# Performance work log

Hardware: AMD Instinct MI355X
Metric: run time of the kernel (lower is better)

Reference implementation:

```python
import jax, jax.numpy as jnp
import numpy as np

B, T, C, H, HD = 4, 2048, 1024, 16, 64

def setup_inputs() -> dict:
    key = jax.random.key(0)
    ks = jax.random.split(key, 9)
    s = 1.0 / np.sqrt(C)
    return {
        "x":  jax.random.normal(ks[0], (B, T, C), jnp.float32),
        "Wq": jax.random.normal(ks[1], (H, C, HD), jnp.float32) * s,
        "bq": jax.random.normal(ks[2], (H, HD), jnp.float32) * 0.02,
        "Wk": jax.random.normal(ks[3], (H, C, HD), jnp.float32) * s,
        "bk": jax.random.normal(ks[4], (H, HD), jnp.float32) * 0.02,
        "Wv": jax.random.normal(ks[5], (H, C, HD), jnp.float32) * s,
        "bv": jax.random.normal(ks[6], (H, HD), jnp.float32) * 0.02,
        "Wo": jax.random.normal(ks[7], (C, C), jnp.float32) * s,
        "bo": jax.random.normal(ks[8], (C,), jnp.float32) * 0.02,
    }

def reference(x, Wq, bq, Wk, bk, Wv, bv, Wo, bo):
    # Batched per-head linear projections: [B,T,C] x [H,C,D] -> [B,H,T,D]
    q = jnp.einsum('btc,hcd->bhtd', x, Wq) + bq[None, :, None, :]
    k = jnp.einsum('btc,hcd->bhtd', x, Wk) + bk[None, :, None, :]
    v = jnp.einsum('btc,hcd->bhtd', x, Wv) + bv[None, :, None, :]
    scale = 1.0 / jnp.sqrt(jnp.asarray(HD, q.dtype))
    scores = jnp.einsum('bhtd,bhsd->bhts', q, k) * scale  # [B,H,T,T]
    causal = jnp.tril(jnp.ones((T, T), dtype=bool))
    scores = jnp.where(causal[None, None, :, :], scores, -jnp.inf)
    attn = jax.nn.softmax(scores, axis=-1)
    out = jnp.einsum('bhts,bhsd->bhtd', attn, v)          # [B,H,T,D]
    concat = out.transpose(0, 2, 1, 3).reshape(B, T, C)   # concat heads
    return concat @ Wo + bo
```

## Files before the change

kernel.cpp:

```cpp
#include <hip/hip_runtime.h>
#include <stdint.h>

#define TSEQ 2048
#define NHEAD 16

typedef __attribute__((ext_vector_type(8))) short bf16x8;
typedef __attribute__((ext_vector_type(4))) short bf16x4;
typedef __attribute__((ext_vector_type(4))) float f32x4;

__device__ __forceinline__ unsigned short f2bf(float f) {
  union { float f; uint32_t u; } c;
  c.f = f;
  uint32_t u = c.u;
  u += 0x7fffu + ((u >> 16) & 1u);
  return (unsigned short)(u >> 16);
}

__device__ __forceinline__ float fexp2(float x) {
#if __has_builtin(__builtin_amdgcn_exp2f)
  return __builtin_amdgcn_exp2f(x);
#else
  return __builtin_exp2f(x);
#endif
}

using as3_void  = __attribute__((address_space(3))) void;
using as1_cvoid = const __attribute__((address_space(1))) void;

__device__ __forceinline__ void gld_lds16(const void* g, void* l) {
  __builtin_amdgcn_global_load_lds((as1_cvoid*)g, (as3_void*)l, 16, 0, 0);
}


__global__ void cast_x_kernel(const float4* __restrict__ x, unsigned short* __restrict__ xb) {
  int i = blockIdx.x * 256 + threadIdx.x;
  float4 v = x[i];
  int e = i * 4;
  int m = e >> 10, k = e & 1023;
  int ks = k ^ ((m & 7) << 3);
  ushort4 o;
  o.x = f2bf(v.x); o.y = f2bf(v.y); o.z = f2bf(v.z); o.w = f2bf(v.w);
  *(ushort4*)(xb + (size_t)m * 1024 + ks) = o;
}

__global__ void repack_wqkv(const float* __restrict__ Wq, const float* __restrict__ Wk,
                            const float* __restrict__ Wv, unsigned short* __restrict__ BT) {
  __shared__ unsigned short tile[64][72];
  const float* W = (blockIdx.z == 0) ? Wq : (blockIdx.z == 1) ? Wk : Wv;
  const int h = blockIdx.y;
  const int c0 = blockIdx.x * 64;
  const int t = threadIdx.x;
  const float* src = W + ((size_t)h * 1024 + c0) * 64;
#pragma unroll
  for (int p = 0; p < 16; ++p) {
    int idx = p * 256 + t;
    int cc = idx >> 6, d = idx & 63;
    tile[cc][d] = f2bf(src[(size_t)cc * 64 + d]);
  }
  __syncthreads();
  unsigned short* dst = BT + ((size_t)blockIdx.z * 1024 + (size_t)h * 64) * 1024 + c0;
#pragma unroll
  for (int p = 0; p < 16; ++p) {
    int idx = p * 256 + t;
    int d = idx >> 6, cc = idx & 63;
    dst[(size_t)d * 1024 + (cc ^ ((d & 7) << 3))] = tile[cc][d];
  }
}

__global__ void repack_wo(const float* __restrict__ Wo, unsigned short* __restrict__ WoT) {
  __shared__ unsigned short tile[64][72];
  const int k0 = blockIdx.x * 64;
  const int n0 = blockIdx.y * 64;
  const int t = threadIdx.x;
#pragma unroll
  for (int p = 0; p < 16; ++p) {
    int idx = p * 256 + t;
    int kk = idx >> 6, nn = idx & 63;
    tile[kk][nn] = f2bf(Wo[(size_t)(k0 + kk) * 1024 + n0 + nn]);
  }
  __syncthreads();
#pragma unroll
  for (int p = 0; p < 16; ++p) {
    int idx = p * 256 + t;
    int nn = idx >> 6, kk = idx & 63;
    WoT[(size_t)(n0 + nn) * 1024 + k0 + (kk ^ ((nn & 7) << 3))] = tile[kk][nn];
  }
}


template <int MODE>
__global__ __launch_bounds__(256) void gemm_bt(
    const unsigned short* __restrict__ A, const unsigned short* __restrict__ BTm,
    const float* __restrict__ bias0, const float* __restrict__ bias1,
    const float* __restrict__ bias2,
    unsigned short* __restrict__ qo, unsigned short* __restrict__ ko,
    unsigned short* __restrict__ vto, float* __restrict__ outf,
    int K, int N) {
  __shared__ __align__(16) char lds[65536];

  const int tid = threadIdx.x, lane = tid & 63, wv = tid >> 6;
  const int wr = wv >> 1, wc = wv & 1;
  const int g = lane >> 4, r = lane & 15;
  const int m0 = blockIdx.x * 128, n0 = blockIdx.y * 128;
  const int xr = (r & 7) << 4;

  f32x4 acc[4][4] = {};

  const int arow = tid >> 3;
  const int acol = (tid & 7) * 8;
  const unsigned short* Ab = A + (size_t)(m0 + arow) * K + acol;
  const unsigned short* Bb = BTm + (size_t)(n0 + arow) * K + acol;

#define GSTAGE(b, kel) do {                                                 \
    char* ab_ = lds + (b) * 32768 + wv * 1024;                              \
    _Pragma("unroll") for (int i = 0; i < 4; ++i) {                         \
      gld_lds16(Ab + (size_t)i * 32 * K + (kel), ab_ + i * 4096);           \
      gld_lds16(Bb + (size_t)i * 32 * K + (kel), ab_ + 16384 + i * 4096);   \
    } } while (0)

  const int NT = K >> 6;
  GSTAGE(0, 0);
  __syncthreads();

  for (int t = 0; t < NT; ++t) {
    const int cur = t & 1;
    if (t + 1 < NT) GSTAGE(cur ^ 1, (t + 1) << 6);
    const char* Ar = lds + cur * 32768;
    const char* Br = Ar + 16384;
#pragma unroll
    for (int kk = 0; kk < 2; ++kk) {
      bf16x8 af[4], bfv[4];
#pragma unroll
      for (int f = 0; f < 4; ++f) {
        af[f]  = *(const bf16x8*)(Ar + (wr * 64 + f * 16 + r) * 128 + ((kk * 64 + g * 16) ^ xr));
        bfv[f] = *(const bf16x8*)(Br + (wc * 64 + f * 16 + r) * 128 + ((kk * 64 + g * 16) ^ xr));
      }
#pragma unroll
      for (int fm = 0; fm < 4; ++fm)
#pragma unroll
        for (int fn = 0; fn < 4; ++fn)
          acc[fm][fn] = __builtin_amdgcn_mfma_f32_16x16x32_bf16(af[fm], bfv[fn], acc[fm][fn], 0, 0, 0);
    }
    __syncthreads();
  }
#undef GSTAGE

  if (MODE == 0) {
    const int which = n0 >> 10;
    const float* bias = (which == 0) ? bias0 : (which == 1) ? bias1 : bias2;
    const float sc = (which == 0) ? 0.18033688011112042f : 1.0f;
    const int b = m0 >> 11;
    const int t0 = m0 & 2047;
    unsigned short* ep = (unsigned short*)lds;

#pragma unroll
    for (int h = 0; h < 2; ++h) {
      const int head = ((n0 & 1023) + h * 64) >> 6;
      const size_t bhb = (size_t)(b * NHEAD + head) * 131072;
      __syncthreads();
      if (wc == h) {
        if (which == 2) {
#pragma unroll
          for (int fn = 0; fn < 4; ++fn) {
            const int d = fn * 16 + r;
            const float bvl = bias[head * 64 + d];
#pragma unroll
            for (int fm = 0; fm < 4; ++fm)
#pragma unroll
              for (int j = 0; j < 4; ++j) {
                const int t = wr * 64 + fm * 16 + 4 * g + j;
                ep[d * 136 + t] = f2bf(acc[fm][fn][j] + bvl);
              }
          }
        } else {
#pragma unroll
          for (int fn = 0; fn < 4; ++fn) {
            const int d = fn * 16 + r;
            const float bvl = bias[head * 64 + d];
#pragma unroll
            for (int fm = 0; fm < 4; ++fm)
#pragma unroll
              for (int j = 0; j < 4; ++j) {
                const int t = wr * 64 + fm * 16 + 4 * g + j;
                ep[t * 72 + d] = f2bf((acc[fm][fn][j] + bvl) * sc);
              }
          }
        }
      }
      __syncthreads();
      if (which == 2) {
#pragma unroll
        for (int p = 0; p < 4; ++p) {
          const int d = p * 16 + (tid >> 4);
          const int u = tid & 15;
          const int c = u >> 3;
          const int w = u & 7;
          const int kk = w >> 2, gg = w & 3;
          const int base_t = c * 64 + kk * 32 + 4 * gg;
          union { bf16x4 h4[2]; bf16x8 v8; } cc2;
          cc2.h4[0] = *(const bf16x4*)(ep + d * 136 + base_t);
          cc2.h4[1] = *(const bf16x4*)(ep + d * 136 + base_t + 16);
          const int q_base = w * 8;
          *(bf16x8*)(vto + bhb + (size_t)((t0 >> 6) + c) * 4096 + (size_t)d * 64 +
                     (q_base ^ ((d & 7) << 3))) = cc2.v8;
        }
      } else {
        unsigned short* qk = (which == 1) ? ko : qo;
#pragma unroll
        for (int p = 0; p < 4; ++p) {
          const int row = p * 32 + (tid >> 3);
          const int seg = tid & 7;
          const bf16x8 v8 = *(const bf16x8*)(ep + row * 72 + seg * 8);
          const int tt = t0 + row;
          int dbase = seg * 8;
          if (which == 1) dbase ^= (tt & 7) << 3;
          *(bf16x8*)(qk + bhb + (size_t)tt * 64 + dbase) = v8;
        }
      }
    }
  } else {
    float* epf = (float*)lds;
#pragma unroll
    for (int h = 0; h < 2; ++h) {
      __syncthreads();
      if (wc == h) {
#pragma unroll
        for (int fn = 0; fn < 4; ++fn) {
          const int n = n0 + h * 64 + fn * 16 + r;
          const float bvl = bias0[n];
#pragma unroll
          for (int fm = 0; fm < 4; ++fm)
#pragma unroll
            for (int j = 0; j < 4; ++j)
              epf[(wr * 64 + fm * 16 + 4 * g + j) * 68 + fn * 16 + r] = acc[fm][fn][j] + bvl;
        }
      }
      __syncthreads();
#pragma unroll
      for (int p = 0; p < 8; ++p) {
        const int row = p * 16 + (tid >> 4);
        const int seg = tid & 15;
        const f32x4 v4 = *(const f32x4*)(epf + row * 68 + seg * 4);
        *(f32x4*)(outf + (size_t)(m0 + row) * N + n0 + h * 64 + seg * 4) = v4;
      }
    }
  }
}


__global__ __launch_bounds__(256) void attn_fwd(const unsigned short* __restrict__ Qm,
                                                const unsigned short* __restrict__ Km,
                                                const unsigned short* __restrict__ Vtm,
                                                unsigned short* __restrict__ Om) {
  __shared__ __align__(16) unsigned short Ks[2][4096];
  __shared__ __align__(16) unsigned short Vs[2][4096];

  const int tid = threadIdx.x, lane = tid & 63, wv = tid >> 6;
  const int g = lane >> 4, r = lane & 15;
  const int bh = blockIdx.x & 63;
  const int p = 31 - (blockIdx.x >> 6);
  const int nt = p + 1;

  const unsigned short* Qp = Qm + (size_t)bh * 131072;
  const unsigned short* Kp = Km + (size_t)bh * 131072;
  const unsigned short* Vp = Vtm + (size_t)bh * 131072;

  const int qb = p * 64 + wv * 16;

  bf16x8 qf[2];
#pragma unroll
  for (int h2 = 0; h2 < 2; ++h2)
    qf[h2] = *(const bf16x8*)(Qp + (size_t)(qb + r) * 64 + h2 * 32 + g * 8);

  f32x4 oacc[4] = {};
  float m_ = -__builtin_inff();
  float l_ = 0.f;

  const uint32_t sw = (uint32_t)((r & 7) << 4);
  const uint32_t ob = (uint32_t)(r * 128);
  const uint32_t c0 = ((uint32_t)(g * 16)) ^ sw;
  const uint32_t c1 = ((uint32_t)(64 + g * 16)) ^ sw;
  const char* const KsB = (const char*)Ks;
  const char* const VsB = (const char*)Vs;

#define ASTAGE(buf, c) do {                                                      \
    const unsigned short* kg_ = Kp + (size_t)(c) * 4096;                         \
    const unsigned short* vg_ = Vp + (size_t)(c) * 4096;                         \
    const int o0_ = wv * 1024;                                                   \
    gld_lds16(kg_ + (o0_ >> 1) + lane * 8, (char*)Ks[buf] + o0_);                \
    gld_lds16(vg_ + (o0_ >> 1) + lane * 8, (char*)Vs[buf] + o0_);                \
    gld_lds16(kg_ + ((o0_ + 4096) >> 1) + lane * 8, (char*)Ks[buf] + o0_ + 4096);\
    gld_lds16(vg_ + ((o0_ + 4096) >> 1) + lane * 8, (char*)Vs[buf] + o0_ + 4096);\
  } while (0)

  ASTAGE(0, 0);
  __syncthreads();

  for (int t = 0; t < nt; ++t) {
    const uint32_t bo = (uint32_t)((t & 1) << 13);
    if (t + 1 < nt) ASTAGE((t & 1) ^ 1, t + 1);

    const char* pk0 = KsB + bo + ob + c0;
    const char* pk1 = KsB + bo + ob + c1;
    const char* pv0 = VsB + bo + ob + c0;
    const char* pv1 = VsB + bo + ob + c1;
    bf16x8 kf[4][2], vf[4][2];
#pragma unroll
    for (int tt = 0; tt < 4; ++tt) {
      kf[tt][0] = *(const bf16x8*)(pk0 + tt * 2048);
      kf[tt][1] = *(const bf16x8*)(pk1 + tt * 2048);
      vf[tt][0] = *(const bf16x8*)(pv0 + tt * 2048);
      vf[tt][1] = *(const bf16x8*)(pv1 + tt * 2048);
    }

    f32x4 sT[4];
    __builtin_amdgcn_s_setprio(1);
#pragma unroll
    for (int tt = 0; tt < 4; ++tt) {
      f32x4 a = {0.f, 0.f, 0.f, 0.f};
      a = __builtin_amdgcn_mfma_f32_16x16x32_bf16(kf[tt][0], qf[0], a, 0, 0, 0);
      a = __builtin_amdgcn_mfma_f32_16x16x32_bf16(kf[tt][1], qf[1], a, 0, 0, 0);
      sT[tt] = a;
    }
    __builtin_amdgcn_s_setprio(0);

    const int qg = qb + r;
    if (t * 64 + 63 > qb) {
#pragma unroll
      for (int tt = 0; tt < 4; ++tt)
#pragma unroll
        for (int j = 0; j < 4; ++j) {
          const int kv = t * 64 + tt * 16 + 4 * g + j;
          sT[tt][j] = (kv <= qg) ? sT[tt][j] : -__builtin_inff();
        }
    }

    float tm[4];
#pragma unroll
    for (int tt = 0; tt < 4; ++tt)
      tm[tt] = fmaxf(fmaxf(sT[tt][0], sT[tt][1]), fmaxf(sT[tt][2], sT[tt][3]));
    const float mx = fmaxf(fmaxf(tm[0], tm[1]), fmaxf(tm[2], tm[3]));

    float mcur = m_;
    const bool norescale = __all(mx <= mcur + 4.0f);
    if (!norescale) {
      float rmx = mx;
      rmx = fmaxf(rmx, __shfl_xor(rmx, 16));
      rmx = fmaxf(rmx, __shfl_xor(rmx, 32));
      const float mnew = fmaxf(mcur, rmx);
      const float rs = fexp2(mcur - mnew);
      m_ = mnew;
      mcur = mnew;
      l_ *= rs;
      float rsb[4];
#pragma unroll
      for (int j = 0; j < 4; ++j) rsb[j] = __shfl(rs, 4 * g + j);
#pragma unroll
      for (int df = 0; df < 4; ++df)
#pragma unroll
        for (int j = 0; j < 4; ++j) oacc[df][j] *= rsb[j];
    }

    float ts = 0.f;
#pragma unroll
    for (int tt = 0; tt < 4; ++tt)
#pragma unroll
      for (int j = 0; j < 4; ++j) {
        const float pp = fexp2(sT[tt][j] - mcur);
        sT[tt][j] = pp;
        ts += pp;
      }
    l_ += ts;

    union { uint32_t w[8]; bf16x8 v[2]; } pu;
#pragma unroll
    for (int tt = 0; tt < 4; ++tt) {
      asm("v_cvt_pk_bf16_f32 %0, %1, %2" : "=v"(pu.w[2 * tt])
          : "v"(sT[tt][0]), "v"(sT[tt][1]));
      asm("v_cvt_pk_bf16_f32 %0, %1, %2" : "=v"(pu.w[2 * tt + 1])
          : "v"(sT[tt][2]), "v"(sT[tt][3]));
    }

    __builtin_amdgcn_s_setprio(1);
#pragma unroll
    for (int kk = 0; kk < 2; ++kk)
#pragma unroll
      for (int df = 0; df < 4; ++df)
        oacc[df] = __builtin_amdgcn_mfma_f32_16x16x32_bf16(pu.v[kk], vf[df][kk], oacc[df], 0, 0, 0);
    __builtin_amdgcn_s_setprio(0);

    __syncthreads();
  }
#undef ASTAGE

  const int b = bh >> 4, h = bh & 15;
  float lt = l_;
  lt += __shfl_xor(lt, 16);
  lt += __shfl_xor(lt, 32);
  float inv[4];
#pragma unroll
  for (int j = 0; j < 4; ++j) {
    const float lb = __shfl(lt, 4 * g + j);
    inv[j] = __builtin_amdgcn_rcpf(lb);
  }
#pragma unroll
  for (int df = 0; df < 4; ++df)
#pragma unroll
    for (int j = 0; j < 4; ++j) {
      const int trow = qb + 4 * g + j;
      const float ov = oacc[df][j] * inv[j];
      const int col = (df * 16 + r) ^ ((trow & 7) << 3);
      Om[((size_t)(b * TSEQ + trow)) * 1024 + h * 64 + col] = f2bf(ov);
    }
}


extern "C" void kernel_launch(void* const* d_in, const int* in_sizes, int n_in,
                              void* d_out, int out_size, void* d_ws, size_t ws_size,
                              hipStream_t stream) {
  const float* x  = (const float*)d_in[0];
  const float* Wq = (const float*)d_in[1];
  const float* bq = (const float*)d_in[2];
  const float* Wk = (const float*)d_in[3];
  const float* bk = (const float*)d_in[4];
  const float* Wv = (const float*)d_in[5];
  const float* bv = (const float*)d_in[6];
  const float* Wo = (const float*)d_in[7];
  const float* bo = (const float*)d_in[8];
  float* out = (float*)d_out;

  unsigned short* xb  = (unsigned short*)d_ws;
  unsigned short* btq = xb + (size_t)8192 * 1024;
  unsigned short* wot = btq + (size_t)3072 * 1024;
  unsigned short* qb  = wot + (size_t)1024 * 1024;
  unsigned short* kb  = qb + (size_t)64 * 2048 * 64;
  unsigned short* vtb = kb + (size_t)64 * 2048 * 64;

  cast_x_kernel<<<8192, 256, 0, stream>>>((const float4*)x, xb);
  repack_wqkv<<<dim3(16, 16, 3), 256, 0, stream>>>(Wq, Wk, Wv, btq);
  repack_wo<<<dim3(16, 16), 256, 0, stream>>>(Wo, wot);

  gemm_bt<0><<<dim3(64, 24), 256, 0, stream>>>(xb, btq, bq, bk, bv, qb, kb, vtb,
                                               nullptr, 1024, 3072);
  attn_fwd<<<2048, 256, 0, stream>>>(qb, kb, vtb, xb);
  gemm_bt<1><<<dim3(64, 8), 256, 0, stream>>>(xb, wot, bo, nullptr, nullptr,
                                              nullptr, nullptr, nullptr, out,
                                              1024, 1024);
}
```

Before: 178.1 us.

## Triple-buffer K/V tiles and software-pipeline QK^T one tile ahead of softmax

The K/V LDS staging goes from double to triple buffering, so global loads are issued two tiles ahead. The loop is also software-pipelined: QK^T for tile t+1 is computed before the softmax and PV of tile t, so MFMA work can overlap with the exp/max VALU work. The cost is more LDS per block (48KB instead of 32KB) and more live registers for the extra score tile, which may reduce occupancy.

After: 180.6 us. About the same (+1.4%).

```diff
diff --git a/kernel.cpp b/kernel.cpp
--- a/kernel.cpp
+++ b/kernel.cpp
@@ -252,8 +252,8 @@
                                                 const unsigned short* __restrict__ Km,
                                                 const unsigned short* __restrict__ Vtm,
                                                 unsigned short* __restrict__ Om) {
-  __shared__ __align__(16) unsigned short Ks[2][4096];
-  __shared__ __align__(16) unsigned short Vs[2][4096];
+  __shared__ __align__(16) unsigned short Ks[3 * 4096];
+  __shared__ __align__(16) unsigned short Vs[3 * 4096];
 
   const int tid = threadIdx.x, lane = tid & 63, wv = tid >> 6;
   const int g = lane >> 4, r = lane & 15;
@@ -283,115 +283,108 @@
   const char* const KsB = (const char*)Ks;
   const char* const VsB = (const char*)Vs;
 
-#define ASTAGE(buf, c) do {                                                      \
+#define ASTAGE(boff, c) do {                                                     \
     const unsigned short* kg_ = Kp + (size_t)(c) * 4096;                         \
     const unsigned short* vg_ = Vp + (size_t)(c) * 4096;                         \
     const int o0_ = wv * 1024;                                                   \
-    gld_lds16(kg_ + (o0_ >> 1) + lane * 8, (char*)Ks[buf] + o0_);                \
-    gld_lds16(vg_ + (o0_ >> 1) + lane * 8, (char*)Vs[buf] + o0_);                \
-    gld_lds16(kg_ + ((o0_ + 4096) >> 1) + lane * 8, (char*)Ks[buf] + o0_ + 4096);\
-    gld_lds16(vg_ + ((o0_ + 4096) >> 1) + lane * 8, (char*)Vs[buf] + o0_ + 4096);\
+    gld_lds16(kg_ + (o0_ >> 1) + lane * 8, (char*)Ks + (boff) + o0_);            \
+    gld_lds16(vg_ + (o0_ >> 1) + lane * 8, (char*)Vs + (boff) + o0_);            \
+    gld_lds16(kg_ + ((o0_ + 4096) >> 1) + lane * 8, (char*)Ks + (boff) + o0_ + 4096); \
+    gld_lds16(vg_ + ((o0_ + 4096) >> 1) + lane * 8, (char*)Vs + (boff) + o0_ + 4096); \
   } while (0)
 
+#define QKT(BOFF, dst) do {                                                      \
+    const char* pk0_ = KsB + (BOFF) + ob + c0;                                   \
+    const char* pk1_ = KsB + (BOFF) + ob + c1;                                   \
+    __builtin_amdgcn_s_setprio(1);                                               \
+    _Pragma("unroll") for (int tt = 0; tt < 4; ++tt) {                           \
+      const bf16x8 k0_ = *(const bf16x8*)(pk0_ + tt * 2048);                     \
+      const bf16x8 k1_ = *(const bf16x8*)(pk1_ + tt * 2048);                     \
+      f32x4 a_ = {0.f, 0.f, 0.f, 0.f};                                           \
+      a_ = __builtin_amdgcn_mfma_f32_16x16x32_bf16(k0_, qf[0], a_, 0, 0, 0);     \
+      a_ = __builtin_amdgcn_mfma_f32_16x16x32_bf16(k1_, qf[1], a_, 0, 0, 0);     \
+      dst[tt] = a_;                                                              \
+    }                                                                            \
+    __builtin_amdgcn_s_setprio(0);                                               \
+  } while (0)
+
+#define SMPV(TI, BOFF) do {                                                      \
+    const int qg_ = qb + r;                                                      \
+    if ((TI) * 64 + 63 > qb) {                                                   \
+      _Pragma("unroll") for (int tt = 0; tt < 4; ++tt)                           \
+      _Pragma("unroll") for (int j = 0; j < 4; ++j) {                            \
+        const int kv_ = (TI) * 64 + tt * 16 + 4 * g + j;                         \
+        sP[tt][j] = (kv_ <= qg_) ? sP[tt][j] : -__builtin_inff();                \
+      }                                                                          \
+    }                                                                            \
+    float tm_[4];                                                                \
+    _Pragma("unroll") for (int tt = 0; tt < 4; ++tt)                             \
+      tm_[tt] = fmaxf(fmaxf(sP[tt][0], sP[tt][1]), fmaxf(sP[tt][2], sP[tt][3])); \
+    const float mx_ = fmaxf(fmaxf(tm_[0], tm_[1]), fmaxf(tm_[2], tm_[3]));       \
+    float mcur_ = m_;                                                            \
+    const bool nors_ = __all(mx_ <= mcur_ + 4.0f);                               \
+    if (!nors_) {                                                                \
+      float rmx_ = mx_;                                                          \
+      rmx_ = fmaxf(rmx_, __shfl_xor(rmx_, 16));                                  \
+      rmx_ = fmaxf(rmx_, __shfl_xor(rmx_, 32));                                  \
+      const float mnew_ = fmaxf(mcur_, rmx_);                                    \
+      const float rs_ = fexp2(mcur_ - mnew_);                                    \
+      m_ = mnew_; mcur_ = mnew_;                                                 \
+      l_ *= rs_;                                                                 \
+      float rsb_[4];                                                             \
+      _Pragma("unroll") for (int j = 0; j < 4; ++j) rsb_[j] = __shfl(rs_, 4 * g + j); \
+      _Pragma("unroll") for (int df = 0; df < 4; ++df)                           \
+      _Pragma("unroll") for (int j = 0; j < 4; ++j) oacc[df][j] *= rsb_[j];      \
+    }                                                                            \
+    float ts_ = 0.f;                                                             \
+    _Pragma("unroll") for (int tt = 0; tt < 4; ++tt)                             \
+    _Pragma("unroll") for (int j = 0; j < 4; ++j) {                              \
+      const float pp_ = fexp2(sP[tt][j] - mcur_);                                \
+      sP[tt][j] = pp_;                                                           \
+      ts_ += pp_;                                                                \
+    }                                                                            \
+    l_ += ts_;                                                                   \
+    union { uint32_t w[8]; bf16x8 v[2]; } pu_;                                   \
+    _Pragma("unroll") for (int tt = 0; tt < 4; ++tt) {                           \
+      asm("v_cvt_pk_bf16_f32 %0, %1, %2" : "=v"(pu_.w[2 * tt])                   \
+          : "v"(sP[tt][0]), "v"(sP[tt][1]));                                     \
+      asm("v_cvt_pk_bf16_f32 %0, %1, %2" : "=v"(pu_.w[2 * tt + 1])               \
+          : "v"(sP[tt][2]), "v"(sP[tt][3]));                                     \
+    }                                                                            \
+    const char* pv0_ = VsB + (BOFF) + ob + c0;                                   \
+    const char* pv1_ = VsB + (BOFF) + ob + c1;                                   \
+    __builtin_amdgcn_s_setprio(1);                                               \
+    _Pragma("unroll") for (int df = 0; df < 4; ++df) {                           \
+      const bf16x8 v0_ = *(const bf16x8*)(pv0_ + df * 2048);                     \
+      const bf16x8 v1_ = *(const bf16x8*)(pv1_ + df * 2048);                     \
+      oacc[df] = __builtin_amdgcn_mfma_f32_16x16x32_bf16(pu_.v[0], v0_, oacc[df], 0, 0, 0); \
+      oacc[df] = __builtin_amdgcn_mfma_f32_16x16x32_bf16(pu_.v[1], v1_, oacc[df], 0, 0, 0); \
+    }                                                                            \
+    __builtin_amdgcn_s_setprio(0);                                               \
+  } while (0)
+
+  f32x4 sP[4], sN[4];
+
   ASTAGE(0, 0);
+  if (nt > 1) ASTAGE(8192, 1);
   __syncthreads();
-
-  for (int t = 0; t < nt; ++t) {
-    const uint32_t bo = (uint32_t)((t & 1) << 13);
-    if (t + 1 < nt) ASTAGE((t & 1) ^ 1, t + 1);
-
-    const char* pk0 = KsB + bo + ob + c0;
-    const char* pk1 = KsB + bo + ob + c1;
-    const char* pv0 = VsB + bo + ob + c0;
-    const char* pv1 = VsB + bo + ob + c1;
-    bf16x8 kf[4][2], vf[4][2];
-#pragma unroll
-    for (int tt = 0; tt < 4; ++tt) {
-      kf[tt][0] = *(const bf16x8*)(pk0 + tt * 2048);
-      kf[tt][1] = *(const bf16x8*)(pk1 + tt * 2048);
-      vf[tt][0] = *(const bf16x8*)(pv0 + tt * 2048);
-      vf[tt][1] = *(const bf16x8*)(pv1 + tt * 2048);
-    }
-
-    f32x4 sT[4];
-    __builtin_amdgcn_s_setprio(1);
-#pragma unroll
-    for (int tt = 0; tt < 4; ++tt) {
-      f32x4 a = {0.f, 0.f, 0.f, 0.f};
-      a = __builtin_amdgcn_mfma_f32_16x16x32_bf16(kf[tt][0], qf[0], a, 0, 0, 0);
-      a = __builtin_amdgcn_mfma_f32_16x16x32_bf16(kf[tt][1], qf[1], a, 0, 0, 0);
-      sT[tt] = a;
-    }
-    __builtin_amdgcn_s_setprio(0);
-
-    const int qg = qb + r;
-    if (t * 64 + 63 > qb) {
-#pragma unroll
-      for (int tt = 0; tt < 4; ++tt)
-#pragma unroll
-        for (int j = 0; j < 4; ++j) {
-          const int kv = t * 64 + tt * 16 + 4 * g + j;
-          sT[tt][j] = (kv <= qg) ? sT[tt][j] : -__builtin_inff();
-        }
-    }
-
-    float tm[4];
-#pragma unroll
-    for (int tt = 0; tt < 4; ++tt)
-      tm[tt] = fmaxf(fmaxf(sT[tt][0], sT[tt][1]), fmaxf(sT[tt][2], sT[tt][3]));
-    const float mx = fmaxf(fmaxf(tm[0], tm[1]), fmaxf(tm[2], tm[3]));
-
-    float mcur = m_;
-    const bool norescale = __all(mx <= mcur + 4.0f);
-    if (!norescale) {
-      float rmx = mx;
-      rmx = fmaxf(rmx, __shfl_xor(rmx, 16));
-      rmx = fmaxf(rmx, __shfl_xor(rmx, 32));
-      const float mnew = fmaxf(mcur, rmx);
-      const float rs = fexp2(mcur - mnew);
-      m_ = mnew;
-      mcur = mnew;
-      l_ *= rs;
-      float rsb[4];
-#pragma unroll
-      for (int j = 0; j < 4; ++j) rsb[j] = __shfl(rs, 4 * g + j);
-#pragma unroll
-      for (int df = 0; df < 4; ++df)
-#pragma unroll
-        for (int j = 0; j < 4; ++j) oacc[df][j] *= rsb[j];
-    }
-
-    float ts = 0.f;
-#pragma unroll
-    for (int tt = 0; tt < 4; ++tt)
-#pragma unroll
-      for (int j = 0; j < 4; ++j) {
-        const float pp = fexp2(sT[tt][j] - mcur);
-        sT[tt][j] = pp;
-        ts += pp;
-      }
-    l_ += ts;
-
-    union { uint32_t w[8]; bf16x8 v[2]; } pu;
-#pragma unroll
-    for (int tt = 0; tt < 4; ++tt) {
-      asm("v_cvt_pk_bf16_f32 %0, %1, %2" : "=v"(pu.w[2 * tt])
-          : "v"(sT[tt][0]), "v"(sT[tt][1]));
-      asm("v_cvt_pk_bf16_f32 %0, %1, %2" : "=v"(pu.w[2 * tt + 1])
-          : "v"(sT[tt][2]), "v"(sT[tt][3]));
-    }
-
-    __builtin_amdgcn_s_setprio(1);
-#pragma unroll
-    for (int kk = 0; kk < 2; ++kk)
-#pragma unroll
-      for (int df = 0; df < 4; ++df)
-        oacc[df] = __builtin_amdgcn_mfma_f32_16x16x32_bf16(pu.v[kk], vf[df][kk], oacc[df], 0, 0, 0);
-    __builtin_amdgcn_s_setprio(0);
-
+  QKT(0, sP);
+
+  uint32_t bCur = 0, bNxt = 8192, bStg = 16384;
+  for (int t = 0; t < nt - 1; ++t) {
+    if (t + 2 < nt) ASTAGE(bStg, t + 2);
+    QKT(bNxt, sN);
+    SMPV(t, bCur);
+#pragma unroll
+    for (int tt = 0; tt < 4; ++tt) sP[tt] = sN[tt];
+    const uint32_t tmp_ = bCur; bCur = bNxt; bNxt = bStg; bStg = tmp_;
     __syncthreads();
   }
+  SMPV(nt - 1, bCur);
+
 #undef ASTAGE
+#undef QKT
+#undef SMPV
 
   const int b = bh >> 4, h = bh & 15;
   float lt = l_;
```
